# Kernel tuning notes

Measured on AMD Instinct MI355X. Metric: run time of the kernel, lower is better.

The kernel has to match this reference:

```python
import jax, jax.numpy as jnp
import numpy as np
from jax import lax

B, T, L = 2048, 80, 128


def setup_inputs() -> dict:
    key = jax.random.key(0)
    k1, k2, k3, k4, k5 = jax.random.split(key, 5)
    x = jax.random.normal(k1, (B, T, L), dtype=jnp.float32)  # emissions (model logits)
    y = jax.random.randint(k2, (B, T), 0, L)                 # gold tag sequence
    trans = jax.random.normal(k3, (L, L), dtype=jnp.float32) * 0.1
    start_trans = jax.random.normal(k4, (L,), dtype=jnp.float32) * 0.1
    end_trans = jax.random.normal(k5, (L,), dtype=jnp.float32) * 0.1
    return {"x": x, "trans": trans, "start_trans": start_trans,
            "end_trans": end_trans, "y": y}


def reference(x, trans, start_trans, end_trans, y):
    # Linear-chain CRF log-likelihood (TorchCRF semantics, mask = all ones).
    # x: [B,T,L] emissions, y: [B,T] gold tags. Returns [B] log-likelihoods.
    # --- numerator: score of the gold path ---
    emit = jnp.take_along_axis(x, y[..., None], axis=2).squeeze(-1).sum(axis=1)  # [B]
    tr = trans[y[:, :-1], y[:, 1:]].sum(axis=1)                                  # [B]
    numerator = start_trans[y[:, 0]] + emit + tr + end_trans[y[:, -1]]           # [B]
    # --- denominator: log-partition via forward algorithm (scan over time) ---
    alpha0 = start_trans[None, :] + x[:, 0]  # [B,L]
    xt = jnp.swapaxes(x, 0, 1)[1:]           # [T-1,B,L]

    def step(alpha, h_t):
        # alpha[b,i] + trans[i,j] -> logsumexp over i, then add emission h_t[b,j]
        a = jax.nn.logsumexp(alpha[:, :, None] + trans[None, :, :], axis=1) + h_t
        return a, None

    alpha, _ = lax.scan(step, alpha0, xt)
    log_z = jax.nn.logsumexp(alpha + end_trans[None, :], axis=1)  # [B]
    return numerator - log_z
```

## Files before the change

kernel.cpp:

```cpp
#include <hip/hip_runtime.h>
#include <math.h>


#define CRF_B 2048
#define CRF_T 80
#define CRF_L 128
#define R_REAL 4

typedef __attribute__((ext_vector_type(8))) short bf16x8_t;
typedef __attribute__((ext_vector_type(4))) float f32x4_t;

__device__ __forceinline__ int pack_bf16_trunc(float lo, float hi) {
    return (int)((__float_as_uint(lo) >> 16) | (__float_as_uint(hi) & 0xFFFF0000u));
}
__device__ __forceinline__ unsigned short bft(float f) {
    return (unsigned short)(__float_as_uint(f) >> 16);
}

__global__ __launch_bounds__(256) void crf_v6_kernel(
    const float* __restrict__ x,
    const float* __restrict__ trans,
    const float* __restrict__ start_trans,
    const float* __restrict__ end_trans,
    const int*   __restrict__ y,
    float* __restrict__ out)
{
    const int tid  = threadIdx.x;
    const int w    = tid >> 6;
    const int lane = tid & 63;
    const int quad = lane >> 4;
    const int n16  = lane & 15;
    const int row0 = blockIdx.x * R_REAL;
    const int brow = row0 + (n16 & (R_REAL - 1));

    __shared__ __attribute__((aligned(16))) short Vb[2][16][136];
    __shared__ __attribute__((aligned(16))) float maxb[16][4];
    __shared__ __attribute__((aligned(16))) float sumb[16][4];
    __shared__ float numb[R_REAL];

    {
        const int bb = row0 + w;
        const int* yb = y + bb * CRF_T;
        const float* xbn = x + (size_t)bb * CRF_T * CRF_L;
        float p = 0.f;
        for (int t = lane; t < CRF_T; t += 64) {
            const int yt = yb[t];
            p += xbn[t * CRF_L + yt];
            p += (t + 1 < CRF_T) ? trans[yt * CRF_L + yb[t + 1]] : end_trans[yt];
            if (t == 0) p += start_trans[yt];
        }
        #pragma unroll
        for (int off = 1; off <= 32; off <<= 1) p += __shfl_xor(p, off);
        if (lane == 0) numb[w] = p;
    }

    bf16x8_t Af[2][4];
    #pragma unroll
    for (int mt = 0; mt < 2; ++mt) {
        const int m = 32 * w + 16 * mt + n16;
        #pragma unroll
        for (int kk = 0; kk < 4; ++kk) {
            union { bf16x8_t v; unsigned short s[8]; } u;
            #pragma unroll
            for (int j = 0; j < 8; ++j) {
                const int k = 32 * kk + 8 * quad + j;
                u.s[j] = bft(__expf(trans[k * CRF_L + m]));
            }
            Af[mt][kk] = u.v;
        }
    }

    const int sc0 = 32 * w + 4 * quad;
    const int sc1 = sc0 + 16;
    const float* xr = x + (size_t)brow * CRF_T * CRF_L;

    f32x4_t ex_end[2], st4[2];
    {
        const f32x4_t e0 = *(const f32x4_t*)&end_trans[sc0];
        const f32x4_t e1 = *(const f32x4_t*)&end_trans[sc1];
        #pragma unroll
        for (int r = 0; r < 4; ++r) {
            ex_end[0][r] = __expf(e0[r]);
            ex_end[1][r] = __expf(e1[r]);
        }
        st4[0] = *(const f32x4_t*)&start_trans[sc0];
        st4[1] = *(const f32x4_t*)&start_trans[sc1];
    }

    f32x4_t P[2];
    float invM = 1.f, crun = 0.f;
    f32x4_t xc[2], xn[2];
    xc[0] = *(const f32x4_t*)&xr[sc0];
    xc[1] = *(const f32x4_t*)&xr[sc1];

    for (int t = 0; t < CRF_T; ++t) {
        if (t + 1 < CRF_T) {
            xn[0] = *(const f32x4_t*)&xr[(t + 1) * CRF_L + sc0];
            xn[1] = *(const f32x4_t*)&xr[(t + 1) * CRF_L + sc1];
        }

        const bool ap = (t > 0) && ((t & 3) == 0);
        if (ap) {
            const f32x4_t mb = *(const f32x4_t*)&maxb[n16][0];
            const float M = fmaxf(fmaxf(mb[0], mb[1]), fmaxf(mb[2], mb[3]));
            crun += __logf(M);
            invM  = __builtin_amdgcn_rcpf(M);
        }

        if (t == 0) {
            #pragma unroll
            for (int r = 0; r < 4; ++r) {
                P[0][r] = __expf(st4[0][r] + xc[0][r]);
                P[1][r] = __expf(st4[1][r] + xc[1][r]);
            }
        } else {
            const short* vrow = &Vb[(t - 1) & 1][n16][0];
            bf16x8_t Bf[4];
            #pragma unroll
            for (int kk = 0; kk < 4; ++kk)
                Bf[kk] = *(const bf16x8_t*)&vrow[32 * kk + 8 * quad];
            #pragma unroll
            for (int mt = 0; mt < 2; ++mt) {
                f32x4_t acc = {0.f, 0.f, 0.f, 0.f};
                #pragma unroll
                for (int kk = 0; kk < 4; ++kk)
                    acc = __builtin_amdgcn_mfma_f32_16x16x32_bf16(Af[mt][kk], Bf[kk], acc, 0, 0, 0);
                #pragma unroll
                for (int r = 0; r < 4; ++r) {
                    float e = __expf(xc[mt][r]);
                    if (ap) e *= invM;
                    P[mt][r] = acc[r] * e;
                }
            }
        }

        if (((t & 3) == 3) && (t < CRF_T - 1)) {
            float g = fmaxf(fmaxf(fmaxf(P[0][0], P[0][1]), fmaxf(P[0][2], P[0][3])),
                            fmaxf(fmaxf(P[1][0], P[1][1]), fmaxf(P[1][2], P[1][3])));
            g = fmaxf(g, __shfl_xor(g, 16));
            g = fmaxf(g, __shfl_xor(g, 32));
            if (lane < 16) maxb[n16][w] = g;
        }

        if (t < CRF_T - 1) {
            short* dst = &Vb[t & 1][n16][0];
            const int d00 = pack_bf16_trunc(P[0][0], P[0][1]);
            const int d01 = pack_bf16_trunc(P[0][2], P[0][3]);
            const int d10 = pack_bf16_trunc(P[1][0], P[1][1]);
            const int d11 = pack_bf16_trunc(P[1][2], P[1][3]);
            *(int2*)&dst[sc0] = make_int2(d00, d01);
            *(int2*)&dst[sc1] = make_int2(d10, d11);
            __syncthreads();
        }

        xc[0] = xn[0];
        xc[1] = xn[1];
    }

    float sv = 0.f;
    #pragma unroll
    for (int mt = 0; mt < 2; ++mt)
    #pragma unroll
    for (int r = 0; r < 4; ++r)
        sv += P[mt][r] * ex_end[mt][r];
    sv += __shfl_xor(sv, 16);
    sv += __shfl_xor(sv, 32);
    if (lane < 16) sumb[n16][w] = sv;
    __syncthreads();
    if (tid < R_REAL) {
        const f32x4_t sb = *(const f32x4_t*)&sumb[tid][0];
        const float S = sb[0] + sb[1] + sb[2] + sb[3];
        out[row0 + tid] = numb[tid] - (crun + __logf(S));
    }
}

extern "C" void kernel_launch(void* const* d_in, const int* in_sizes, int n_in,
                              void* d_out, int out_size, void* d_ws, size_t ws_size,
                              hipStream_t stream) {
    const float* x     = (const float*)d_in[0];
    const float* trans = (const float*)d_in[1];
    const float* st    = (const float*)d_in[2];
    const float* et    = (const float*)d_in[3];
    const int*   y     = (const int*)d_in[4];
    float* out = (float*)d_out;

    crf_v6_kernel<<<CRF_B / R_REAL, 256, 0, stream>>>(x, trans, st, et, y, out);
}
```

Measured before the change: 164.3 us.

## Run forward and backward CRF recursions simultaneously and meet in the middle

```diff
diff --git a/kernel.cpp b/kernel.cpp
--- a/kernel.cpp
+++ b/kernel.cpp
@@ -17,7 +17,7 @@
     return (unsigned short)(__float_as_uint(f) >> 16);
 }
 
-__global__ __launch_bounds__(256) void crf_v6_kernel(
+__global__ __launch_bounds__(256, 2) void crf_v8_kernel(
     const float* __restrict__ x,
     const float* __restrict__ trans,
     const float* __restrict__ start_trans,
@@ -33,8 +33,10 @@
     const int row0 = blockIdx.x * R_REAL;
     const int brow = row0 + (n16 & (R_REAL - 1));
 
-    __shared__ __attribute__((aligned(16))) short Vb[2][16][136];
-    __shared__ __attribute__((aligned(16))) float maxb[16][4];
+    __shared__ __attribute__((aligned(16))) short VbF[2][16][136];
+    __shared__ __attribute__((aligned(16))) short VbB[2][16][136];
+    __shared__ __attribute__((aligned(16))) float maxbF[16][4];
+    __shared__ __attribute__((aligned(16))) float maxbB[16][4];
     __shared__ __attribute__((aligned(16))) float sumb[16][4];
     __shared__ float numb[R_REAL];
 
@@ -54,19 +56,21 @@
         if (lane == 0) numb[w] = p;
     }
 
-    bf16x8_t Af[2][4];
+    bf16x8_t AfF[2][4], AfB[2][4];
     #pragma unroll
     for (int mt = 0; mt < 2; ++mt) {
         const int m = 32 * w + 16 * mt + n16;
         #pragma unroll
         for (int kk = 0; kk < 4; ++kk) {
-            union { bf16x8_t v; unsigned short s[8]; } u;
+            union { bf16x8_t v; unsigned short s[8]; } uF, uB;
             #pragma unroll
             for (int j = 0; j < 8; ++j) {
                 const int k = 32 * kk + 8 * quad + j;
-                u.s[j] = bft(__expf(trans[k * CRF_L + m]));
-            }
-            Af[mt][kk] = u.v;
+                uF.s[j] = bft(__expf(trans[k * CRF_L + m]));
+                uB.s[j] = bft(__expf(trans[m * CRF_L + k]));
+            }
+            AfF[mt][kk] = uF.v;
+            AfB[mt][kk] = uB.v;
         }
     }
 
@@ -74,95 +78,155 @@
     const int sc1 = sc0 + 16;
     const float* xr = x + (size_t)brow * CRF_T * CRF_L;
 
-    f32x4_t ex_end[2], st4[2];
+    f32x4_t PF[2], PB[2];
+    float invF = 1.f, crunF = 0.f, invB = 1.f, crunB = 0.f;
+
     {
-        const f32x4_t e0 = *(const f32x4_t*)&end_trans[sc0];
-        const f32x4_t e1 = *(const f32x4_t*)&end_trans[sc1];
+        const f32x4_t st0 = *(const f32x4_t*)&start_trans[sc0];
+        const f32x4_t st1 = *(const f32x4_t*)&start_trans[sc1];
+        const f32x4_t en0 = *(const f32x4_t*)&end_trans[sc0];
+        const f32x4_t en1 = *(const f32x4_t*)&end_trans[sc1];
+        const f32x4_t xf0 = *(const f32x4_t*)&xr[0 * CRF_L + sc0];
+        const f32x4_t xf1 = *(const f32x4_t*)&xr[0 * CRF_L + sc1];
+        const f32x4_t xb0 = *(const f32x4_t*)&xr[79 * CRF_L + sc0];
+        const f32x4_t xb1 = *(const f32x4_t*)&xr[79 * CRF_L + sc1];
         #pragma unroll
         for (int r = 0; r < 4; ++r) {
-            ex_end[0][r] = __expf(e0[r]);
-            ex_end[1][r] = __expf(e1[r]);
-        }
-        st4[0] = *(const f32x4_t*)&start_trans[sc0];
-        st4[1] = *(const f32x4_t*)&start_trans[sc1];
-    }
-
-    f32x4_t P[2];
-    float invM = 1.f, crun = 0.f;
-    f32x4_t xc[2], xn[2];
-    xc[0] = *(const f32x4_t*)&xr[sc0];
-    xc[1] = *(const f32x4_t*)&xr[sc1];
-
-    for (int t = 0; t < CRF_T; ++t) {
-        if (t + 1 < CRF_T) {
-            xn[0] = *(const f32x4_t*)&xr[(t + 1) * CRF_L + sc0];
-            xn[1] = *(const f32x4_t*)&xr[(t + 1) * CRF_L + sc1];
-        }
-
-        const bool ap = (t > 0) && ((t & 3) == 0);
+            PF[0][r] = __expf(st0[r] + xf0[r]);
+            PF[1][r] = __expf(st1[r] + xf1[r]);
+            PB[0][r] = __expf(en0[r] + xb0[r]);
+            PB[1][r] = __expf(en1[r] + xb1[r]);
+        }
+        short* dF = &VbF[0][n16][0];
+        short* dB = &VbB[0][n16][0];
+        *(int2*)&dF[sc0] = make_int2(pack_bf16_trunc(PF[0][0], PF[0][1]),
+                                     pack_bf16_trunc(PF[0][2], PF[0][3]));
+        *(int2*)&dF[sc1] = make_int2(pack_bf16_trunc(PF[1][0], PF[1][1]),
+                                     pack_bf16_trunc(PF[1][2], PF[1][3]));
+        *(int2*)&dB[sc0] = make_int2(pack_bf16_trunc(PB[0][0], PB[0][1]),
+                                     pack_bf16_trunc(PB[0][2], PB[0][3]));
+        *(int2*)&dB[sc1] = make_int2(pack_bf16_trunc(PB[1][0], PB[1][1]),
+                                     pack_bf16_trunc(PB[1][2], PB[1][3]));
+        __syncthreads();
+    }
+
+    f32x4_t xfc[2], xbc[2], xfn[2], xbn[2];
+    xfc[0] = *(const f32x4_t*)&xr[1 * CRF_L + sc0];
+    xfc[1] = *(const f32x4_t*)&xr[1 * CRF_L + sc1];
+    xbc[0] = *(const f32x4_t*)&xr[78 * CRF_L + sc0];
+    xbc[1] = *(const f32x4_t*)&xr[78 * CRF_L + sc1];
+
+    for (int k = 1; k <= 39; ++k) {
+        if (k < 39) {
+            xfn[0] = *(const f32x4_t*)&xr[(k + 1) * CRF_L + sc0];
+            xfn[1] = *(const f32x4_t*)&xr[(k + 1) * CRF_L + sc1];
+            xbn[0] = *(const f32x4_t*)&xr[(78 - k) * CRF_L + sc0];
+            xbn[1] = *(const f32x4_t*)&xr[(78 - k) * CRF_L + sc1];
+        }
+
+        const bool ap = (k & 3) == 0;
         if (ap) {
-            const f32x4_t mb = *(const f32x4_t*)&maxb[n16][0];
-            const float M = fmaxf(fmaxf(mb[0], mb[1]), fmaxf(mb[2], mb[3]));
-            crun += __logf(M);
-            invM  = __builtin_amdgcn_rcpf(M);
-        }
-
-        if (t == 0) {
+            const f32x4_t mF = *(const f32x4_t*)&maxbF[n16][0];
+            const f32x4_t mB = *(const f32x4_t*)&maxbB[n16][0];
+            const float MF = fmaxf(fmaxf(mF[0], mF[1]), fmaxf(mF[2], mF[3]));
+            const float MB = fmaxf(fmaxf(mB[0], mB[1]), fmaxf(mB[2], mB[3]));
+            crunF += __logf(MF);  invF = __builtin_amdgcn_rcpf(MF);
+            crunB += __logf(MB);  invB = __builtin_amdgcn_rcpf(MB);
+        }
+
+        float eF[2][4], eB[2][4];
+        #pragma unroll
+        for (int mt = 0; mt < 2; ++mt)
+        #pragma unroll
+        for (int r = 0; r < 4; ++r) {
+            float vF = __expf(xfc[mt][r]);
+            float vB = __expf(xbc[mt][r]);
+            if (ap) { vF *= invF; vB *= invB; }
+            eF[mt][r] = vF;
+            eB[mt][r] = vB;
+        }
+
+        const short* vrF = &VbF[(k - 1) & 1][n16][0];
+        const short* vrB = &VbB[(k - 1) & 1][n16][0];
+        bf16x8_t BfF[4], BfB[4];
+        #pragma unroll
+        for (int kk = 0; kk < 4; ++kk) {
+            BfF[kk] = *(const bf16x8_t*)&vrF[32 * kk + 8 * quad];
+            BfB[kk] = *(const bf16x8_t*)&vrB[32 * kk + 8 * quad];
+        }
+
+        #pragma unroll
+        for (int mt = 0; mt < 2; ++mt) {
+            f32x4_t aF = {0.f, 0.f, 0.f, 0.f};
+            f32x4_t aB = {0.f, 0.f, 0.f, 0.f};
+            #pragma unroll
+            for (int kk = 0; kk < 4; ++kk) {
+                aF = __builtin_amdgcn_mfma_f32_16x16x32_bf16(AfF[mt][kk], BfF[kk], aF, 0, 0, 0);
+                aB = __builtin_amdgcn_mfma_f32_16x16x32_bf16(AfB[mt][kk], BfB[kk], aB, 0, 0, 0);
+            }
             #pragma unroll
             for (int r = 0; r < 4; ++r) {
-                P[0][r] = __expf(st4[0][r] + xc[0][r]);
-                P[1][r] = __expf(st4[1][r] + xc[1][r]);
-            }
+                PF[mt][r] = aF[r] * eF[mt][r];
+                PB[mt][r] = aB[r] * eB[mt][r];
+            }
+        }
+
+        if (((k & 3) == 3) && (k < 39)) {
+            float gF = PF[0][0], gB = PB[0][0];
+            #pragma unroll
+            for (int mt = 0; mt < 2; ++mt)
+            #pragma unroll
+            for (int r = 0; r < 4; ++r) {
+                gF = fmaxf(gF, PF[mt][r]);
+                gB = fmaxf(gB, PB[mt][r]);
+            }
+            gF = fmaxf(gF, __shfl_xor(gF, 16)); gF = fmaxf(gF, __shfl_xor(gF, 32));
+            gB = fmaxf(gB, __shfl_xor(gB, 16)); gB = fmaxf(gB, __shfl_xor(gB, 32));
+            if (lane < 16) { maxbF[n16][w] = gF; maxbB[n16][w] = gB; }
+        }
+
+        if (k < 39) {
+            short* dF = &VbF[k & 1][n16][0];
+            short* dB = &VbB[k & 1][n16][0];
+            *(int2*)&dF[sc0] = make_int2(pack_bf16_trunc(PF[0][0], PF[0][1]),
+                                         pack_bf16_trunc(PF[0][2], PF[0][3]));
+            *(int2*)&dF[sc1] = make_int2(pack_bf16_trunc(PF[1][0], PF[1][1]),
+                                         pack_bf16_trunc(PF[1][2], PF[1][3]));
+            *(int2*)&dB[sc0] = make_int2(pack_bf16_trunc(PB[0][0], PB[0][1]),
+                                         pack_bf16_trunc(PB[0][2], PB[0][3]));
+            *(int2*)&dB[sc1] = make_int2(pack_bf16_trunc(PB[1][0], PB[1][1]),
+                                         pack_bf16_trunc(PB[1][2], PB[1][3]));
         } else {
-            const short* vrow = &Vb[(t - 1) & 1][n16][0];
-            bf16x8_t Bf[4];
+            short* dB = &VbB[1][n16][0];
+            *(int2*)&dB[sc0] = make_int2(pack_bf16_trunc(PB[0][0], PB[0][1]),
+                                         pack_bf16_trunc(PB[0][2], PB[0][3]));
+            *(int2*)&dB[sc1] = make_int2(pack_bf16_trunc(PB[1][0], PB[1][1]),
+                                         pack_bf16_trunc(PB[1][2], PB[1][3]));
+        }
+        __syncthreads();
+
+        xfc[0] = xfn[0]; xfc[1] = xfn[1];
+        xbc[0] = xbn[0]; xbc[1] = xbn[1];
+    }
+
+    float sv = 0.f;
+    {
+        const short* vrB = &VbB[1][n16][0];
+        bf16x8_t BfB[4];
+        #pragma unroll
+        for (int kk = 0; kk < 4; ++kk)
+            BfB[kk] = *(const bf16x8_t*)&vrB[32 * kk + 8 * quad];
+        #pragma unroll
+        for (int mt = 0; mt < 2; ++mt) {
+            f32x4_t aW = {0.f, 0.f, 0.f, 0.f};
             #pragma unroll
             for (int kk = 0; kk < 4; ++kk)
-                Bf[kk] = *(const bf16x8_t*)&vrow[32 * kk + 8 * quad];
-            #pragma unroll
-            for (int mt = 0; mt < 2; ++mt) {
-                f32x4_t acc = {0.f, 0.f, 0.f, 0.f};
-                #pragma unroll
-                for (int kk = 0; kk < 4; ++kk)
-                    acc = __builtin_amdgcn_mfma_f32_16x16x32_bf16(Af[mt][kk], Bf[kk], acc, 0, 0, 0);
-                #pragma unroll
-                for (int r = 0; r < 4; ++r) {
-                    float e = __expf(xc[mt][r]);
-                    if (ap) e *= invM;
-                    P[mt][r] = acc[r] * e;
-                }
-            }
-        }
-
-        if (((t & 3) == 3) && (t < CRF_T - 1)) {
-            float g = fmaxf(fmaxf(fmaxf(P[0][0], P[0][1]), fmaxf(P[0][2], P[0][3])),
-                            fmaxf(fmaxf(P[1][0], P[1][1]), fmaxf(P[1][2], P[1][3])));
-            g = fmaxf(g, __shfl_xor(g, 16));
-            g = fmaxf(g, __shfl_xor(g, 32));
-            if (lane < 16) maxb[n16][w] = g;
-        }
-
-        if (t < CRF_T - 1) {
-            short* dst = &Vb[t & 1][n16][0];
-            const int d00 = pack_bf16_trunc(P[0][0], P[0][1]);
-            const int d01 = pack_bf16_trunc(P[0][2], P[0][3]);
-            const int d10 = pack_bf16_trunc(P[1][0], P[1][1]);
-            const int d11 = pack_bf16_trunc(P[1][2], P[1][3]);
-            *(int2*)&dst[sc0] = make_int2(d00, d01);
-            *(int2*)&dst[sc1] = make_int2(d10, d11);
-            __syncthreads();
-        }
-
-        xc[0] = xn[0];
-        xc[1] = xn[1];
-    }
-
-    float sv = 0.f;
-    #pragma unroll
-    for (int mt = 0; mt < 2; ++mt)
-    #pragma unroll
-    for (int r = 0; r < 4; ++r)
-        sv += P[mt][r] * ex_end[mt][r];
+                aW = __builtin_amdgcn_mfma_f32_16x16x32_bf16(AfB[mt][kk], BfB[kk], aW, 0, 0, 0);
+            #pragma unroll
+            for (int r = 0; r < 4; ++r)
+                sv += PF[mt][r] * aW[r];
+        }
+    }
     sv += __shfl_xor(sv, 16);
     sv += __shfl_xor(sv, 32);
     if (lane < 16) sumb[n16][w] = sv;
@@ -170,7 +234,7 @@
     if (tid < R_REAL) {
         const f32x4_t sb = *(const f32x4_t*)&sumb[tid][0];
         const float S = sb[0] + sb[1] + sb[2] + sb[3];
-        out[row0 + tid] = numb[tid] - (crun + __logf(S));
+        out[row0 + tid] = numb[tid] - (crunF + crunB + __logf(S));
     }
 }
 
@@ -184,5 +248,5 @@
     const int*   y     = (const int*)d_in[4];
     float* out = (float*)d_out;
 
-    crf_v6_kernel<<<CRF_B / R_REAL, 256, 0, stream>>>(x, trans, st, et, y, out);
-}
+    crf_v8_kernel<<<CRF_B / R_REAL, 256, 0, stream>>>(x, trans, st, et, y, out);
+}
```

Measured after the change: 157.0 us. 4.4% less time.

## Split CRF forward recursion into concurrent forward and backward halves

Applied to the files above, without the earlier changes.

```diff
diff --git a/kernel.cpp b/kernel.cpp
--- a/kernel.cpp
+++ b/kernel.cpp
@@ -6,18 +6,22 @@
 #define CRF_T 80
 #define CRF_L 128
 #define R_REAL 4
+#define VSTRIDE 144
 
 typedef __attribute__((ext_vector_type(8))) short bf16x8_t;
 typedef __attribute__((ext_vector_type(4))) float f32x4_t;
 
-__device__ __forceinline__ int pack_bf16_trunc(float lo, float hi) {
-    return (int)((__float_as_uint(lo) >> 16) | (__float_as_uint(hi) & 0xFFFF0000u));
+__device__ __forceinline__ int pk(float lo, float hi) {
+    return __builtin_amdgcn_perm(__float_as_int(hi), __float_as_int(lo), 0x07060302);
 }
 __device__ __forceinline__ unsigned short bft(float f) {
     return (unsigned short)(__float_as_uint(f) >> 16);
 }
-
-__global__ __launch_bounds__(256) void crf_v6_kernel(
+__device__ __forceinline__ float bf2f(unsigned short s) {
+    return __uint_as_float(((unsigned)s) << 16);
+}
+
+__global__ __launch_bounds__(256, 2) void crf_v9_kernel(
     const float* __restrict__ x,
     const float* __restrict__ trans,
     const float* __restrict__ start_trans,
@@ -33,9 +37,15 @@
     const int row0 = blockIdx.x * R_REAL;
     const int brow = row0 + (n16 & (R_REAL - 1));
 
-    __shared__ __attribute__((aligned(16))) short Vb[2][16][136];
-    __shared__ __attribute__((aligned(16))) float maxb[16][4];
-    __shared__ __attribute__((aligned(16))) float sumb[16][4];
+    const bool isF  = (w < 2);
+    const int  half = w & 1;
+    const int  mb   = 64 * half;
+
+    __shared__ __attribute__((aligned(16))) short VbF[2][16][VSTRIDE];
+    __shared__ __attribute__((aligned(16))) short VbB[2][16][VSTRIDE];
+    __shared__ __attribute__((aligned(16))) float maxb[2][16][2];
+    __shared__ __attribute__((aligned(16))) float sumb[16][2];
+    __shared__ float cb[16];
     __shared__ float numb[R_REAL];
 
     {
@@ -54,123 +64,166 @@
         if (lane == 0) numb[w] = p;
     }
 
-    bf16x8_t Af[2][4];
+    bf16x8_t Af[4][4];
     #pragma unroll
-    for (int mt = 0; mt < 2; ++mt) {
-        const int m = 32 * w + 16 * mt + n16;
+    for (int mt = 0; mt < 4; ++mt) {
+        const int m = mb + 16 * mt + n16;
         #pragma unroll
         for (int kk = 0; kk < 4; ++kk) {
             union { bf16x8_t v; unsigned short s[8]; } u;
             #pragma unroll
             for (int j = 0; j < 8; ++j) {
                 const int k = 32 * kk + 8 * quad + j;
-                u.s[j] = bft(__expf(trans[k * CRF_L + m]));
+                u.s[j] = bft(__expf(isF ? trans[k * CRF_L + m]
+                                        : trans[m * CRF_L + k]));
             }
             Af[mt][kk] = u.v;
         }
     }
 
-    const int sc0 = 32 * w + 4 * quad;
-    const int sc1 = sc0 + 16;
     const float* xr = x + (size_t)brow * CRF_T * CRF_L;
-
-    f32x4_t ex_end[2], st4[2];
+    const int ci = isF ? 0 : 1;
+    short (*Vw)[16][VSTRIDE] = isF ? VbF : VbB;
+
+    f32x4_t P[4];
+    float invM = 1.f, crun = 0.f;
+
     {
-        const f32x4_t e0 = *(const f32x4_t*)&end_trans[sc0];
-        const f32x4_t e1 = *(const f32x4_t*)&end_trans[sc1];
-        #pragma unroll
-        for (int r = 0; r < 4; ++r) {
-            ex_end[0][r] = __expf(e0[r]);
-            ex_end[1][r] = __expf(e1[r]);
-        }
-        st4[0] = *(const f32x4_t*)&start_trans[sc0];
-        st4[1] = *(const f32x4_t*)&start_trans[sc1];
-    }
-
-    f32x4_t P[2];
-    float invM = 1.f, crun = 0.f;
-    f32x4_t xc[2], xn[2];
-    xc[0] = *(const f32x4_t*)&xr[sc0];
-    xc[1] = *(const f32x4_t*)&xr[sc1];
-
-    for (int t = 0; t < CRF_T; ++t) {
-        if (t + 1 < CRF_T) {
-            xn[0] = *(const f32x4_t*)&xr[(t + 1) * CRF_L + sc0];
-            xn[1] = *(const f32x4_t*)&xr[(t + 1) * CRF_L + sc1];
-        }
-
-        const bool ap = (t > 0) && ((t & 3) == 0);
-        if (ap) {
-            const f32x4_t mb = *(const f32x4_t*)&maxb[n16][0];
-            const float M = fmaxf(fmaxf(mb[0], mb[1]), fmaxf(mb[2], mb[3]));
+        const int t0 = isF ? 0 : 79;
+        const float* bt = isF ? start_trans : end_trans;
+        #pragma unroll
+        for (int mt = 0; mt < 4; ++mt) {
+            const int sc = mb + 16 * mt + 4 * quad;
+            const f32x4_t b4 = *(const f32x4_t*)&bt[sc];
+            const f32x4_t x4 = *(const f32x4_t*)&xr[t0 * CRF_L + sc];
+            #pragma unroll
+            for (int r = 0; r < 4; ++r)
+                P[mt][r] = __expf(b4[r] + x4[r]);
+        }
+        short* dst = &Vw[0][n16][0];
+        #pragma unroll
+        for (int mt = 0; mt < 4; ++mt) {
+            const int sc = mb + 16 * mt + 4 * quad;
+            *(int2*)&dst[sc] = make_int2(pk(P[mt][0], P[mt][1]),
+                                         pk(P[mt][2], P[mt][3]));
+        }
+        __syncthreads();
+    }
+
+    f32x4_t xc[4], xn[4];
+    {
+        const int t1 = isF ? 1 : 78;
+        #pragma unroll
+        for (int mt = 0; mt < 4; ++mt)
+            xc[mt] = *(const f32x4_t*)&xr[t1 * CRF_L + mb + 16 * mt + 4 * quad];
+    }
+
+    auto step = [&](int k, const bool AP, const bool MX, const bool PRE) {
+        if (PRE) {
+            const int tn = isF ? (k + 1) : (78 - k);
+            #pragma unroll
+            for (int mt = 0; mt < 4; ++mt)
+                xn[mt] = *(const f32x4_t*)&xr[tn * CRF_L + mb + 16 * mt + 4 * quad];
+        }
+        if (AP) {
+            const float2 mv = *(const float2*)&maxb[ci][n16][0];
+            const float M = fmaxf(mv.x, mv.y);
             crun += __logf(M);
             invM  = __builtin_amdgcn_rcpf(M);
         }
-
-        if (t == 0) {
-            #pragma unroll
-            for (int r = 0; r < 4; ++r) {
-                P[0][r] = __expf(st4[0][r] + xc[0][r]);
-                P[1][r] = __expf(st4[1][r] + xc[1][r]);
-            }
-        } else {
-            const short* vrow = &Vb[(t - 1) & 1][n16][0];
-            bf16x8_t Bf[4];
+        float e[4][4];
+        #pragma unroll
+        for (int mt = 0; mt < 4; ++mt)
+        #pragma unroll
+        for (int r = 0; r < 4; ++r) {
+            float ev = __expf(xc[mt][r]);
+            if (AP) ev *= invM;
+            e[mt][r] = ev;
+        }
+        const short* vrow = &Vw[(k - 1) & 1][n16][0];
+        bf16x8_t Bf[4];
+        #pragma unroll
+        for (int kk = 0; kk < 4; ++kk)
+            Bf[kk] = *(const bf16x8_t*)&vrow[32 * kk + 8 * quad];
+        #pragma unroll
+        for (int mt = 0; mt < 4; ++mt) {
+            f32x4_t a = {0.f, 0.f, 0.f, 0.f};
             #pragma unroll
             for (int kk = 0; kk < 4; ++kk)
-                Bf[kk] = *(const bf16x8_t*)&vrow[32 * kk + 8 * quad];
-            #pragma unroll
-            for (int mt = 0; mt < 2; ++mt) {
-                f32x4_t acc = {0.f, 0.f, 0.f, 0.f};
-                #pragma unroll
-                for (int kk = 0; kk < 4; ++kk)
-                    acc = __builtin_amdgcn_mfma_f32_16x16x32_bf16(Af[mt][kk], Bf[kk], acc, 0, 0, 0);
-                #pragma unroll
-                for (int r = 0; r < 4; ++r) {
-                    float e = __expf(xc[mt][r]);
-                    if (ap) e *= invM;
-                    P[mt][r] = acc[r] * e;
-                }
-            }
-        }
-
-        if (((t & 3) == 3) && (t < CRF_T - 1)) {
-            float g = fmaxf(fmaxf(fmaxf(P[0][0], P[0][1]), fmaxf(P[0][2], P[0][3])),
-                            fmaxf(fmaxf(P[1][0], P[1][1]), fmaxf(P[1][2], P[1][3])));
+                a = __builtin_amdgcn_mfma_f32_16x16x32_bf16(Af[mt][kk], Bf[kk], a, 0, 0, 0);
+            #pragma unroll
+            for (int r = 0; r < 4; ++r)
+                P[mt][r] = a[r] * e[mt][r];
+        }
+        if (MX) {
+            float g = P[0][0];
+            #pragma unroll
+            for (int mt = 0; mt < 4; ++mt)
+            #pragma unroll
+            for (int r = 0; r < 4; ++r)
+                g = fmaxf(g, P[mt][r]);
             g = fmaxf(g, __shfl_xor(g, 16));
             g = fmaxf(g, __shfl_xor(g, 32));
-            if (lane < 16) maxb[n16][w] = g;
-        }
-
-        if (t < CRF_T - 1) {
-            short* dst = &Vb[t & 1][n16][0];
-            const int d00 = pack_bf16_trunc(P[0][0], P[0][1]);
-            const int d01 = pack_bf16_trunc(P[0][2], P[0][3]);
-            const int d10 = pack_bf16_trunc(P[1][0], P[1][1]);
-            const int d11 = pack_bf16_trunc(P[1][2], P[1][3]);
-            *(int2*)&dst[sc0] = make_int2(d00, d01);
-            *(int2*)&dst[sc1] = make_int2(d10, d11);
-            __syncthreads();
-        }
-
-        xc[0] = xn[0];
-        xc[1] = xn[1];
-    }
-
-    float sv = 0.f;
-    #pragma unroll
-    for (int mt = 0; mt < 2; ++mt)
-    #pragma unroll
-    for (int r = 0; r < 4; ++r)
-        sv += P[mt][r] * ex_end[mt][r];
-    sv += __shfl_xor(sv, 16);
-    sv += __shfl_xor(sv, 32);
-    if (lane < 16) sumb[n16][w] = sv;
+            if (lane < 16) maxb[ci][n16][half] = g;
+        }
+        short* dst = &Vw[k & 1][n16][0];
+        #pragma unroll
+        for (int mt = 0; mt < 4; ++mt) {
+            const int sc = mb + 16 * mt + 4 * quad;
+            *(int2*)&dst[sc] = make_int2(pk(P[mt][0], P[mt][1]),
+                                         pk(P[mt][2], P[mt][3]));
+        }
+        __syncthreads();
+        #pragma unroll
+        for (int mt = 0; mt < 4; ++mt) xc[mt] = xn[mt];
+    };
+
+    step(1, false, false, true);
+    step(2, false, false, true);
+    step(3, false, true,  true);
+    for (int g = 1; g <= 8; ++g) {
+        const int k = 4 * g;
+        step(k,     true,  false, true);
+        step(k + 1, false, false, true);
+        step(k + 2, false, false, true);
+        step(k + 3, false, true,  true);
+    }
+    step(36, true,  false, true);
+    step(37, false, false, true);
+    step(38, false, false, true);
+    step(39, false, false, false);
+
+    if (isF) {
+        const short* vrow = &VbF[1][n16][0];
+        bf16x8_t Bf[4];
+        #pragma unroll
+        for (int kk = 0; kk < 4; ++kk)
+            Bf[kk] = *(const bf16x8_t*)&vrow[32 * kk + 8 * quad];
+        float sv = 0.f;
+        #pragma unroll
+        for (int mt = 0; mt < 4; ++mt) {
+            f32x4_t a = {0.f, 0.f, 0.f, 0.f};
+            #pragma unroll
+            for (int kk = 0; kk < 4; ++kk)
+                a = __builtin_amdgcn_mfma_f32_16x16x32_bf16(Af[mt][kk], Bf[kk], a, 0, 0, 0);
+            const int sc = mb + 16 * mt + 4 * quad;
+            const int2 v2 = *(const int2*)&VbB[1][n16][sc];
+            sv += a[0] * bf2f((unsigned short)(v2.x & 0xFFFF));
+            sv += a[1] * bf2f((unsigned short)(((unsigned)v2.x) >> 16));
+            sv += a[2] * bf2f((unsigned short)(v2.y & 0xFFFF));
+            sv += a[3] * bf2f((unsigned short)(((unsigned)v2.y) >> 16));
+        }
+        sv += __shfl_xor(sv, 16);
+        sv += __shfl_xor(sv, 32);
+        if (lane < 16) sumb[n16][half] = sv;
+    } else {
+        if (w == 2 && lane < 16) cb[n16] = crun;
+    }
     __syncthreads();
     if (tid < R_REAL) {
-        const f32x4_t sb = *(const f32x4_t*)&sumb[tid][0];
-        const float S = sb[0] + sb[1] + sb[2] + sb[3];
-        out[row0 + tid] = numb[tid] - (crun + __logf(S));
+        const float2 sb = *(const float2*)&sumb[tid][0];
+        const float S = sb.x + sb.y;
+        out[row0 + tid] = numb[tid] - (crun + cb[tid] + __logf(S));
     }
 }
 
@@ -184,5 +237,5 @@
     const int*   y     = (const int*)d_in[4];
     float* out = (float*)d_out;
 
-    crf_v6_kernel<<<CRF_B / R_REAL, 256, 0, stream>>>(x, trans, st, et, y, out);
-}
+    crf_v9_kernel<<<CRF_B / R_REAL, 256, 0, stream>>>(x, trans, st, et, y, out);
+}
```

Result: slower. 170.8 us (+3.9%).
